# Kernel tuning notes

Hardware: AMD Instinct MI355X
Metric: run time of the kernel (lower is better)

Reference implementation:

```python
import jax, jax.numpy as jnp
import numpy as np

N_NODES = 50000

def gcn_conv(x, src, dst, W, b):
    # x: [N, F_in], src/dst: [E], W: [F_in, F_out], b: [F_out]
    n = x.shape[0]
    xw = x @ W  # [N, F_out]
    # degree including self-loop (counted on destination nodes, PyG convention)
    deg = jax.ops.segment_sum(jnp.ones(src.shape[0], xw.dtype), dst, num_segments=n) + 1.0
    dinv = jax.lax.rsqrt(deg)  # deg >= 1 always
    norm = dinv[src] * dinv[dst]  # [E]
    msgs = xw[src] * norm[:, None]  # [E, F_out] gather + scale
    agg = jax.ops.segment_sum(msgs, dst, num_segments=n)  # scatter-add
    agg = agg + xw * (dinv * dinv)[:, None]  # self-loop contribution
    return agg + b


def setup_inputs() -> dict:
    key = jax.random.key(0)
    ks = jax.random.split(key, 8)
    n, e = N_NODES, 800000
    c_in, c_hid, c_out = 128, 128, 64
    x = jax.random.normal(ks[0], (n, c_in), dtype=jnp.float32)
    edge_index = jax.random.randint(ks[1], (2, e), 0, n, dtype=jnp.int64)
    s = 1.0 / np.sqrt(c_in)
    W1 = jax.random.uniform(ks[2], (c_in, c_hid), jnp.float32, -s, s)
    b1 = jnp.zeros((c_hid,), jnp.float32)
    sh = 1.0 / np.sqrt(c_hid)
    W2 = jax.random.uniform(ks[3], (c_hid, c_hid), jnp.float32, -sh, sh)
    b2 = jnp.zeros((c_hid,), jnp.float32)
    W3 = jax.random.uniform(ks[4], (c_hid, c_out), jnp.float32, -sh, sh)
    b3 = jnp.zeros((c_out,), jnp.float32)
    return {"x": x, "edge_index": edge_index, "W1": W1, "b1": b1,
            "W2": W2, "b2": b2, "W3": W3, "b3": b3}


def reference(x, edge_index, W1, b1, W2, b2, W3, b3):
    src, dst = edge_index[0], edge_index[1]
    h = gcn_conv(x, src, dst, W1, b1)
    h = gcn_conv(h, src, dst, W2, b2)
    h = gcn_conv(h, src, dst, W3, b3)
    return jax.nn.relu(h)  # activation applied after last layer only
```

## Files before the change

### kernel.cpp

```cpp
#include <hip/hip_runtime.h>
#include <hip/hip_fp16.h>


#define C_IN 128
#define C_HID 128
#define C_OUT 64
#define PART_BLOCKS 256

typedef __attribute__((ext_vector_type(8))) short bf16x8;
typedef __attribute__((ext_vector_type(4))) float f32x4;

__device__ __forceinline__ unsigned short bf16_rne(float f) {
    unsigned u = __float_as_uint(f);
    unsigned r = u + 0x7FFFu + ((u >> 16) & 1u);
    return (unsigned short)(r >> 16);
}
__device__ __forceinline__ float bf16_f(unsigned short h) {
    return __uint_as_float(((unsigned)h) << 16);
}


__global__ __launch_bounds__(256) void buk_hist_kernel(const int* __restrict__ dst, int E,
                                                       int* __restrict__ bukCnt) {
    __shared__ int h[256];
    int tid = threadIdx.x;
    h[tid] = 0;
    __syncthreads();
    int chunk = (E + gridDim.x - 1) / gridDim.x;
    int lo = blockIdx.x * chunk;
    int hi = min(lo + chunk, E);
    for (int e = lo + tid; e < hi; e += 256)
        atomicAdd(&h[dst[e] >> 8], 1);
    __syncthreads();
    if (h[tid] > 0) atomicAdd(&bukCnt[tid], h[tid]);
}

__global__ __launch_bounds__(256) void buk_scan_kernel(const int* __restrict__ bukCnt,
                                                       int nbuk, int E,
                                                       int* __restrict__ bbase,
                                                       int* __restrict__ cursor) {
    __shared__ int lds[256];
    int tid = threadIdx.x;
    int v = (tid < nbuk) ? bukCnt[tid] : 0;
    lds[tid] = v;
    __syncthreads();
    for (int off = 1; off < 256; off <<= 1) {
        int u = (tid >= off) ? lds[tid - off] : 0;
        __syncthreads();
        lds[tid] += u;
        __syncthreads();
    }
    int ex = lds[tid] - v;
    if (tid < nbuk) { bbase[tid] = ex; cursor[tid] = ex; }
    if (tid == 0) bbase[nbuk] = E;
}

__global__ __launch_bounds__(256) void buk_place_kernel(const int* __restrict__ src,
                                                        const int* __restrict__ dst, int E,
                                                        int* __restrict__ cursor,
                                                        int2* __restrict__ ebuf) {
    __shared__ int h[256];
    __shared__ int base[256];
    __shared__ int c2[256];
    int tid = threadIdx.x;
    h[tid] = 0;
    c2[tid] = 0;
    __syncthreads();
    int chunk = (E + gridDim.x - 1) / gridDim.x;
    int lo = blockIdx.x * chunk;
    int hi = min(lo + chunk, E);
    for (int e = lo + tid; e < hi; e += 256)
        atomicAdd(&h[dst[e] >> 8], 1);
    __syncthreads();
    int cnt = h[tid];
    if (cnt > 0) base[tid] = atomicAdd(&cursor[tid], cnt);
    __syncthreads();
    for (int e = lo + tid; e < hi; e += 256) {
        int d = dst[e];
        int b = d >> 8;
        int slot = base[b] + atomicAdd(&c2[b], 1);
        ebuf[slot] = make_int2(src[e], d);
    }
}

__global__ __launch_bounds__(256) void buk_fill_kernel(const int2* __restrict__ ebuf,
                                                       const int* __restrict__ bbase,
                                                       int n, int E,
                                                       int* __restrict__ rowptr,
                                                       float* __restrict__ dinv,
                                                       int* __restrict__ csr) {
    __shared__ int deg[256];
    __shared__ int lds[256];
    int b = blockIdx.x;
    int tid = threadIdx.x;
    int lo = bbase[b];
    int hi = bbase[b + 1];
    int node0 = b << 8;
    deg[tid] = 0;
    __syncthreads();
    for (int e = lo + tid; e < hi; e += 256)
        atomicAdd(&deg[ebuf[e].y & 255], 1);
    __syncthreads();
    int d = deg[tid];
    lds[tid] = d;
    __syncthreads();
    for (int off = 1; off < 256; off <<= 1) {
        int u = (tid >= off) ? lds[tid - off] : 0;
        __syncthreads();
        lds[tid] += u;
        __syncthreads();
    }
    int ex = lds[tid] - d;
    int node = node0 + tid;
    if (node < n) {
        rowptr[node] = lo + ex;
        dinv[node] = rsqrtf((float)d + 1.0f);
    }
    if (tid == 0)
        rowptr[min(node0 + 256, n)] = hi;
    __syncthreads();
    deg[tid] = lo + ex;
    __syncthreads();
    for (int e = lo + tid; e < hi; e += 256) {
        int2 ed = ebuf[e];
        int slot = atomicAdd(&deg[ed.y & 255], 1);
        csr[slot] = ed.x;
    }
}

__global__ __launch_bounds__(256) void split_kernel(const float* __restrict__ X,
                                                    unsigned short* __restrict__ Hi,
                                                    unsigned short* __restrict__ Lo,
                                                    int total4) {
    int g = blockIdx.x * blockDim.x + threadIdx.x;
    if (g >= total4) return;
    float4 v = ((const float4*)X)[g];
    float vv[4] = {v.x, v.y, v.z, v.w};
    unsigned short h[4], l[4];
#pragma unroll
    for (int i = 0; i < 4; ++i) {
        h[i] = bf16_rne(vv[i]);
        l[i] = bf16_rne(vv[i] - bf16_f(h[i]));
    }
    uint2 ph = make_uint2((unsigned)h[0] | ((unsigned)h[1] << 16),
                          (unsigned)h[2] | ((unsigned)h[3] << 16));
    uint2 pl = make_uint2((unsigned)l[0] | ((unsigned)l[1] << 16),
                          (unsigned)l[2] | ((unsigned)l[3] << 16));
    ((uint2*)Hi)[g] = ph;
    ((uint2*)Lo)[g] = pl;
}

__global__ __launch_bounds__(256) void wsplit_all_kernel(const float* __restrict__ W1,
                                                         const float* __restrict__ W2,
                                                         const float* __restrict__ W3,
                                                         unsigned short* __restrict__ Wf) {
    int g = blockIdx.x * 256 + threadIdx.x;
    const float* W;
    int FOUT, NF, base;
    if (g < 2048)      { W = W1; FOUT = 128; NF = 2048; base = 0;     }
    else if (g < 4096) { W = W2; FOUT = 128; NF = 2048; base = 32768; g -= 2048; }
    else if (g < 5120) { W = W3; FOUT = 64;  NF = 1024; base = 65536; g -= 4096; }
    else return;
    int lane = g & 63;
    int nt = (g >> 6) & 3;
    int kt = (g >> 8) & 3;
    int ct = g >> 10;
    int kbase = kt * 32 + (lane >> 4) * 8;
    int cc = ct * 64 + nt * 16 + (lane & 15);
    unsigned short hi8[8], lo8[8];
#pragma unroll
    for (int j = 0; j < 8; ++j) {
        float w = W[(size_t)(kbase + j) * FOUT + cc];
        hi8[j] = bf16_rne(w);
        lo8[j] = bf16_rne(w - bf16_f(hi8[j]));
    }
    *(bf16x8*)&Wf[(size_t)(base + g * 8)] = *(bf16x8*)hi8;
    *(bf16x8*)&Wf[(size_t)(base + NF * 8 + g * 8)] = *(bf16x8*)lo8;
}

template <int FOUT>
__global__ __launch_bounds__(256, 3) void gemm_mfma(const unsigned short* __restrict__ Xhi,
                                                    const unsigned short* __restrict__ Xlo,
                                                    const unsigned short* __restrict__ WfHi,
                                                    const unsigned short* __restrict__ WfLo,
                                                    const float* __restrict__ dinv,
                                                    float* __restrict__ Y,
                                                    __half* __restrict__ Yh, int n) {
    constexpr int CTILES = FOUT / 64;
    int tid = threadIdx.x;
    int wv = tid >> 6, lane = tid & 63;
    int ct = (CTILES == 1) ? 0 : (blockIdx.x % CTILES);
    int rt = blockIdx.x / CTILES;
    int col0 = ct * 64;
    int row0 = rt * 64 + wv * 16;

    int rA = row0 + (lane & 15);
    if (rA > n - 1) rA = n - 1;
    const unsigned short* ph = Xhi + (size_t)rA * 128 + ((lane >> 4) * 8);
    const unsigned short* pl = Xlo + (size_t)rA * 128 + ((lane >> 4) * 8);
    bf16x8 ah[4], al[4];
#pragma unroll
    for (int kt = 0; kt < 4; ++kt) {
        ah[kt] = *(const bf16x8*)(ph + kt * 32);
        al[kt] = *(const bf16x8*)(pl + kt * 32);
    }

    const bf16x8* bhp = (const bf16x8*)WfHi + (size_t)ct * 1024 + lane;
    const bf16x8* blp = (const bf16x8*)WfLo + (size_t)ct * 1024 + lane;

    f32x4 acc[4];
#pragma unroll
    for (int nt = 0; nt < 4; ++nt) acc[nt] = (f32x4){0.f, 0.f, 0.f, 0.f};

#pragma unroll
    for (int kt = 0; kt < 4; ++kt) {
        bf16x8 bh[4], bl[4];
#pragma unroll
        for (int nt = 0; nt < 4; ++nt) {
            bh[nt] = bhp[(kt * 4 + nt) * 64];
            bl[nt] = blp[(kt * 4 + nt) * 64];
        }
#pragma unroll
        for (int nt = 0; nt < 4; ++nt) {
            acc[nt] = __builtin_amdgcn_mfma_f32_16x16x32_bf16(ah[kt], bh[nt], acc[nt], 0, 0, 0);
            acc[nt] = __builtin_amdgcn_mfma_f32_16x16x32_bf16(ah[kt], bl[nt], acc[nt], 0, 0, 0);
            acc[nt] = __builtin_amdgcn_mfma_f32_16x16x32_bf16(al[kt], bh[nt], acc[nt], 0, 0, 0);
        }
    }

#pragma unroll
    for (int r = 0; r < 4; ++r) {
        int grow = row0 + (lane >> 4) * 4 + r;
        if (grow < n) {
            float di = dinv[grow];
#pragma unroll
            for (int nt = 0; nt < 4; ++nt) {
                float v = acc[nt][r];
                size_t off = (size_t)grow * FOUT + col0 + nt * 16 + (lane & 15);
                Y[off] = v;
                Yh[off] = __float2half(v * di);
            }
        }
    }
}

template <int NB, bool MASK>
__device__ __forceinline__ void batch_f128(const int* __restrict__ csr, int j, int rem,
                                           const __half* __restrict__ xwh, int lane,
                                           float2* acc) {
    int s[NB];
#pragma unroll
    for (int k = 0; k < NB; ++k) {
        int jj = MASK ? (j + ((k < rem) ? k : 0)) : (j + k);
        s[k] = csr[jj];
    }
    float2 v[NB];
#pragma unroll
    for (int k = 0; k < NB; ++k) {
        __half2 hv = ((const __half2*)(xwh + (size_t)s[k] * 128))[lane];
        v[k] = __half22float2(hv);
    }
#pragma unroll
    for (int k = 0; k < NB; ++k) {
        float m = (!MASK || (k < rem)) ? 1.0f : 0.0f;
        acc[k & 3].x = fmaf(v[k].x, m, acc[k & 3].x);
        acc[k & 3].y = fmaf(v[k].y, m, acc[k & 3].y);
    }
}

template <int NB, bool MASK>
__device__ __forceinline__ void batch_f64(const int* __restrict__ csr, int j, int rem,
                                          const __half* __restrict__ xwh, int lane,
                                          float* acc) {
    int s[NB];
#pragma unroll
    for (int k = 0; k < NB; ++k) {
        int jj = MASK ? (j + ((k < rem) ? k : 0)) : (j + k);
        s[k] = csr[jj];
    }
    float v[NB];
#pragma unroll
    for (int k = 0; k < NB; ++k)
        v[k] = __half2float(xwh[(size_t)s[k] * 64 + lane]);
#pragma unroll
    for (int k = 0; k < NB; ++k) {
        float m = (!MASK || (k < rem)) ? 1.0f : 0.0f;
        acc[k & 3] = fmaf(v[k], m, acc[k & 3]);
    }
}

template <int F, int MODE>
__global__ __launch_bounds__(256) void agg_kernel(const int* __restrict__ rowptr,
                                                  const int* __restrict__ csr,
                                                  const float* __restrict__ xw,
                                                  const __half* __restrict__ xwh,
                                                  const float* __restrict__ dinv,
                                                  const float* __restrict__ bias,
                                                  float* __restrict__ out,
                                                  unsigned short* __restrict__ outHi,
                                                  unsigned short* __restrict__ outLo,
                                                  int n) {
    int wave = threadIdx.x >> 6;
    int lane = threadIdx.x & 63;
    int i0 = blockIdx.x * 4 + wave;
    if (i0 >= n) return;
    int i = __builtin_amdgcn_readfirstlane(i0);
    float di = dinv[i];
    float d2 = di * di;
    int j = rowptr[i];
    int end = rowptr[i + 1];
    j = __builtin_amdgcn_readfirstlane(j);
    end = __builtin_amdgcn_readfirstlane(end);

    if constexpr (F == 128) {
        float2 x0 = ((const float2*)(xw + (size_t)i * F))[lane];
        float2 acc[4];
        acc[0] = acc[1] = acc[2] = acc[3] = make_float2(0.f, 0.f);

        for (; j + 16 <= end; j += 16) batch_f128<16, false>(csr, j, 0, xwh, lane, acc);
        if (j + 8 <= end) { batch_f128<8, false>(csr, j, 0, xwh, lane, acc); j += 8; }
        if (j + 4 <= end) { batch_f128<4, false>(csr, j, 0, xwh, lane, acc); j += 4; }
        int rem = end - j;
        if (rem > 0) batch_f128<4, true>(csr, j, rem, xwh, lane, acc);

        float2 bv = ((const float2*)bias)[lane];
        float ox = fmaf(di, (acc[0].x + acc[1].x) + (acc[2].x + acc[3].x),
                        fmaf(x0.x, d2, bv.x));
        float oy = fmaf(di, (acc[0].y + acc[1].y) + (acc[2].y + acc[3].y),
                        fmaf(x0.y, d2, bv.y));
        unsigned short h0 = bf16_rne(ox);
        unsigned short l0 = bf16_rne(ox - bf16_f(h0));
        unsigned short h1 = bf16_rne(oy);
        unsigned short l1 = bf16_rne(oy - bf16_f(h1));
        ((unsigned*)(outHi + (size_t)i * F))[lane] = (unsigned)h0 | ((unsigned)h1 << 16);
        ((unsigned*)(outLo + (size_t)i * F))[lane] = (unsigned)l0 | ((unsigned)l1 << 16);
    } else {
        float x0 = xw[(size_t)i * F + lane];
        float acc[4] = {0.f, 0.f, 0.f, 0.f};

        for (; j + 16 <= end; j += 16) batch_f64<16, false>(csr, j, 0, xwh, lane, acc);
        if (j + 8 <= end) { batch_f64<8, false>(csr, j, 0, xwh, lane, acc); j += 8; }
        if (j + 4 <= end) { batch_f64<4, false>(csr, j, 0, xwh, lane, acc); j += 4; }
        int rem = end - j;
        if (rem > 0) batch_f64<4, true>(csr, j, rem, xwh, lane, acc);

        float o = fmaf(di, (acc[0] + acc[1]) + (acc[2] + acc[3]),
                       fmaf(x0, d2, bias[lane]));
        o = fmaxf(o, 0.f);
        out[(size_t)i * F + lane] = o;
    }
}

extern "C" void kernel_launch(void* const* d_in, const int* in_sizes, int n_in,
                              void* d_out, int out_size, void* d_ws, size_t ws_size,
                              hipStream_t stream) {
    const float* x  = (const float*)d_in[0];
    const int*   ei = (const int*)d_in[1];
    const float* W1 = (const float*)d_in[2];
    const float* b1 = (const float*)d_in[3];
    const float* W2 = (const float*)d_in[4];
    const float* b2 = (const float*)d_in[5];
    const float* W3 = (const float*)d_in[6];
    const float* b3 = (const float*)d_in[7];
    float* out = (float*)d_out;

    int E = in_sizes[1] / 2;
    int n = in_sizes[0] / C_IN;
    const int* src = ei;
    const int* dst = ei + E;
    int nbuk = (n + 255) >> 8;

    float*          A    = (float*)d_ws;
    __half*         Ah   = (__half*)(A + (size_t)n * C_HID);
    unsigned short* Bhi  = (unsigned short*)(Ah + (size_t)n * C_HID);
    unsigned short* Blo  = Bhi + (size_t)n * C_HID;
    unsigned short* Wf   = Blo + (size_t)n * C_HID;
    int2*           ebuf = (int2*)(Wf + 81920);
    int*            csr  = (int*)(ebuf + E);
    float*          dinv = (float*)(csr + E);
    int*            rowptr = (int*)(dinv + n);
    int*            bukCnt = rowptr + n + 1;
    int*            bbase  = bukCnt + 256;
    int*            cursor = bbase + 256 + 1;

    unsigned short* W1h = Wf;
    unsigned short* W1l = Wf + 16384;
    unsigned short* W2h = Wf + 32768;
    unsigned short* W2l = Wf + 49152;
    unsigned short* W3h = Wf + 65536;
    unsigned short* W3l = Wf + 73728;

    hipMemsetAsync(bukCnt, 0, 256 * sizeof(int), stream);
    buk_hist_kernel<<<PART_BLOCKS, 256, 0, stream>>>(dst, E, bukCnt);
    buk_scan_kernel<<<1, 256, 0, stream>>>(bukCnt, nbuk, E, bbase, cursor);
    buk_place_kernel<<<PART_BLOCKS, 256, 0, stream>>>(src, dst, E, cursor, ebuf);
    buk_fill_kernel<<<nbuk, 256, 0, stream>>>(ebuf, bbase, n, E, rowptr, dinv, csr);

    wsplit_all_kernel<<<20, 256, 0, stream>>>(W1, W2, W3, Wf);
    int total4 = n * C_IN / 4;
    split_kernel<<<(total4 + 255) / 256, 256, 0, stream>>>(x, Bhi, Blo, total4);

    int aggBlocks = (n + 3) / 4;
    int rowTiles = (n + 63) / 64;

    gemm_mfma<C_HID><<<rowTiles * 2, 256, 0, stream>>>(Bhi, Blo, W1h, W1l, dinv, A, Ah, n);
    agg_kernel<C_HID, 0><<<aggBlocks, 256, 0, stream>>>(rowptr, csr, A, Ah, dinv, b1,
                                                        nullptr, Bhi, Blo, n);
    gemm_mfma<C_HID><<<rowTiles * 2, 256, 0, stream>>>(Bhi, Blo, W2h, W2l, dinv, A, Ah, n);
    agg_kernel<C_HID, 0><<<aggBlocks, 256, 0, stream>>>(rowptr, csr, A, Ah, dinv, b2,
                                                        nullptr, Bhi, Blo, n);
    gemm_mfma<C_OUT><<<rowTiles, 256, 0, stream>>>(Bhi, Blo, W3h, W3l, dinv, A, Ah, n);
    agg_kernel<C_OUT, 1><<<aggBlocks, 256, 0, stream>>>(rowptr, csr, A, Ah, dinv, b3,
                                                        out, nullptr, nullptr, n);
}
```

Before: 278.3 us.

## Fuse aggregation with next-layer GEMM and fold input bf16 split into GEMM1

Drops the standalone split kernel: the first GEMM now reads fp32 x and splits it into bf16 hi/lo in registers. Each layer-1 and layer-2 aggregation is fused with the following layer's MFMA GEMM. Aggregated rows go into a 64-row LDS tile and are multiplied directly, so the hi/lo activation buffers are never written to or re-read from global memory. This removes two launches and intermediate traffic. In exchange each block runs only 4 waves over 64 nodes with a 33KB LDS tile, which lowers parallelism and latency hiding for the irregular gather phase. It also double-buffers the Y arrays.

```diff
diff --git a/kernel.cpp b/kernel.cpp
--- a/kernel.cpp
+++ b/kernel.cpp
@@ -126,28 +126,6 @@
         int slot = atomicAdd(&deg[ed.y & 255], 1);
         csr[slot] = ed.x;
     }
-}
-
-__global__ __launch_bounds__(256) void split_kernel(const float* __restrict__ X,
-                                                    unsigned short* __restrict__ Hi,
-                                                    unsigned short* __restrict__ Lo,
-                                                    int total4) {
-    int g = blockIdx.x * blockDim.x + threadIdx.x;
-    if (g >= total4) return;
-    float4 v = ((const float4*)X)[g];
-    float vv[4] = {v.x, v.y, v.z, v.w};
-    unsigned short h[4], l[4];
-#pragma unroll
-    for (int i = 0; i < 4; ++i) {
-        h[i] = bf16_rne(vv[i]);
-        l[i] = bf16_rne(vv[i] - bf16_f(h[i]));
-    }
-    uint2 ph = make_uint2((unsigned)h[0] | ((unsigned)h[1] << 16),
-                          (unsigned)h[2] | ((unsigned)h[3] << 16));
-    uint2 pl = make_uint2((unsigned)l[0] | ((unsigned)l[1] << 16),
-                          (unsigned)l[2] | ((unsigned)l[3] << 16));
-    ((uint2*)Hi)[g] = ph;
-    ((uint2*)Lo)[g] = pl;
 }
 
 __global__ __launch_bounds__(256) void wsplit_all_kernel(const float* __restrict__ W1,
@@ -178,31 +156,39 @@
     *(bf16x8*)&Wf[(size_t)(base + NF * 8 + g * 8)] = *(bf16x8*)lo8;
 }
 
-template <int FOUT>
-__global__ __launch_bounds__(256, 3) void gemm_mfma(const unsigned short* __restrict__ Xhi,
-                                                    const unsigned short* __restrict__ Xlo,
-                                                    const unsigned short* __restrict__ WfHi,
-                                                    const unsigned short* __restrict__ WfLo,
-                                                    const float* __restrict__ dinv,
-                                                    float* __restrict__ Y,
-                                                    __half* __restrict__ Yh, int n) {
-    constexpr int CTILES = FOUT / 64;
+__device__ __forceinline__ void split8(const float* v, bf16x8& hv, bf16x8& lv) {
+#pragma unroll
+    for (int j = 0; j < 8; ++j) {
+        unsigned short h = bf16_rne(v[j]);
+        hv[j] = (short)h;
+        lv[j] = (short)bf16_rne(v[j] - bf16_f(h));
+    }
+}
+
+__global__ __launch_bounds__(256, 3) void gemm1_mfma(const float* __restrict__ X,
+                                                     const unsigned short* __restrict__ WfHi,
+                                                     const unsigned short* __restrict__ WfLo,
+                                                     const float* __restrict__ dinv,
+                                                     float* __restrict__ Y,
+                                                     __half* __restrict__ Yh, int n) {
+    constexpr int FOUT = 128;
     int tid = threadIdx.x;
     int wv = tid >> 6, lane = tid & 63;
-    int ct = (CTILES == 1) ? 0 : (blockIdx.x % CTILES);
-    int rt = blockIdx.x / CTILES;
+    int ct = blockIdx.x & 1;
+    int rt = blockIdx.x >> 1;
     int col0 = ct * 64;
     int row0 = rt * 64 + wv * 16;
 
     int rA = row0 + (lane & 15);
     if (rA > n - 1) rA = n - 1;
-    const unsigned short* ph = Xhi + (size_t)rA * 128 + ((lane >> 4) * 8);
-    const unsigned short* pl = Xlo + (size_t)rA * 128 + ((lane >> 4) * 8);
+    const float* px = X + (size_t)rA * 128 + ((lane >> 4) * 8);
     bf16x8 ah[4], al[4];
 #pragma unroll
     for (int kt = 0; kt < 4; ++kt) {
-        ah[kt] = *(const bf16x8*)(ph + kt * 32);
-        al[kt] = *(const bf16x8*)(pl + kt * 32);
+        float v[8];
+        *(float4*)&v[0] = *(const float4*)(px + kt * 32);
+        *(float4*)&v[4] = *(const float4*)(px + kt * 32 + 4);
+        split8(v, ah[kt], al[kt]);
     }
 
     const bf16x8* bhp = (const bf16x8*)WfHi + (size_t)ct * 1024 + lane;
@@ -289,17 +275,114 @@
     }
 }
 
-template <int F, int MODE>
-__global__ __launch_bounds__(256) void agg_kernel(const int* __restrict__ rowptr,
-                                                  const int* __restrict__ csr,
-                                                  const float* __restrict__ xw,
-                                                  const __half* __restrict__ xwh,
-                                                  const float* __restrict__ dinv,
-                                                  const float* __restrict__ bias,
-                                                  float* __restrict__ out,
-                                                  unsigned short* __restrict__ outHi,
-                                                  unsigned short* __restrict__ outLo,
-                                                  int n) {
+template <int FOUT>
+__global__ __launch_bounds__(256, 3) void fused_agg_gemm(const int* __restrict__ rowptr,
+                                                         const int* __restrict__ csr,
+                                                         const float* __restrict__ xw,
+                                                         const __half* __restrict__ xwh,
+                                                         const float* __restrict__ dinv,
+                                                         const float* __restrict__ bias,
+                                                         const unsigned short* __restrict__ WfHi,
+                                                         const unsigned short* __restrict__ WfLo,
+                                                         float* __restrict__ Y,
+                                                         __half* __restrict__ Yh, int n) {
+    constexpr int CTILES = FOUT / 64;
+    __shared__ float hl[64][132];
+
+    int tid = threadIdx.x;
+    int wv = tid >> 6, lane = tid & 63;
+    int node0 = blockIdx.x * 64;
+
+    for (int nn = 0; nn < 16; ++nn) {
+        int nodeLocal = wv * 16 + nn;
+        int i0 = node0 + nodeLocal;
+        if (i0 >= n) {
+            ((float2*)&hl[nodeLocal][0])[lane] = make_float2(0.f, 0.f);
+            continue;
+        }
+        int i = __builtin_amdgcn_readfirstlane(i0);
+        float di = dinv[i];
+        float d2 = di * di;
+        int j = rowptr[i];
+        int end = rowptr[i + 1];
+        j = __builtin_amdgcn_readfirstlane(j);
+        end = __builtin_amdgcn_readfirstlane(end);
+
+        float2 x0 = ((const float2*)(xw + (size_t)i * 128))[lane];
+        float2 acc[4];
+        acc[0] = acc[1] = acc[2] = acc[3] = make_float2(0.f, 0.f);
+        for (; j + 16 <= end; j += 16) batch_f128<16, false>(csr, j, 0, xwh, lane, acc);
+        if (j + 8 <= end) { batch_f128<8, false>(csr, j, 0, xwh, lane, acc); j += 8; }
+        if (j + 4 <= end) { batch_f128<4, false>(csr, j, 0, xwh, lane, acc); j += 4; }
+        int rem = end - j;
+        if (rem > 0) batch_f128<4, true>(csr, j, rem, xwh, lane, acc);
+
+        float2 bv = ((const float2*)bias)[lane];
+        float2 o;
+        o.x = fmaf(di, (acc[0].x + acc[1].x) + (acc[2].x + acc[3].x),
+                   fmaf(x0.x, d2, bv.x));
+        o.y = fmaf(di, (acc[0].y + acc[1].y) + (acc[2].y + acc[3].y),
+                   fmaf(x0.y, d2, bv.y));
+        ((float2*)&hl[nodeLocal][0])[lane] = o;
+    }
+
+    int rowL = wv * 16 + (lane & 15);
+    bf16x8 ah[4], al[4];
+#pragma unroll
+    for (int kt = 0; kt < 4; ++kt) {
+        int cb = kt * 32 + (lane >> 4) * 8;
+        float v[8];
+        *(float4*)&v[0] = *(const float4*)&hl[rowL][cb];
+        *(float4*)&v[4] = *(const float4*)&hl[rowL][cb + 4];
+        split8(v, ah[kt], al[kt]);
+    }
+
+#pragma unroll
+    for (int ct = 0; ct < CTILES; ++ct) {
+        const bf16x8* bhp = (const bf16x8*)WfHi + (size_t)ct * 1024 + lane;
+        const bf16x8* blp = (const bf16x8*)WfLo + (size_t)ct * 1024 + lane;
+        f32x4 acc[4];
+#pragma unroll
+        for (int nt = 0; nt < 4; ++nt) acc[nt] = (f32x4){0.f, 0.f, 0.f, 0.f};
+#pragma unroll
+        for (int kt = 0; kt < 4; ++kt) {
+            bf16x8 bh[4], bl[4];
+#pragma unroll
+            for (int nt = 0; nt < 4; ++nt) {
+                bh[nt] = bhp[(kt * 4 + nt) * 64];
+                bl[nt] = blp[(kt * 4 + nt) * 64];
+            }
+#pragma unroll
+            for (int nt = 0; nt < 4; ++nt) {
+                acc[nt] = __builtin_amdgcn_mfma_f32_16x16x32_bf16(ah[kt], bh[nt], acc[nt], 0, 0, 0);
+                acc[nt] = __builtin_amdgcn_mfma_f32_16x16x32_bf16(ah[kt], bl[nt], acc[nt], 0, 0, 0);
+                acc[nt] = __builtin_amdgcn_mfma_f32_16x16x32_bf16(al[kt], bh[nt], acc[nt], 0, 0, 0);
+            }
+        }
+#pragma unroll
+        for (int r = 0; r < 4; ++r) {
+            int grow = node0 + wv * 16 + (lane >> 4) * 4 + r;
+            if (grow < n) {
+                float di = dinv[grow];
+#pragma unroll
+                for (int nt = 0; nt < 4; ++nt) {
+                    float v = acc[nt][r];
+                    size_t off = (size_t)grow * FOUT + ct * 64 + nt * 16 + (lane & 15);
+                    Y[off] = v;
+                    Yh[off] = __float2half(v * di);
+                }
+            }
+        }
+    }
+}
+
+__global__ __launch_bounds__(256) void agg64_kernel(const int* __restrict__ rowptr,
+                                                    const int* __restrict__ csr,
+                                                    const float* __restrict__ xw,
+                                                    const __half* __restrict__ xwh,
+                                                    const float* __restrict__ dinv,
+                                                    const float* __restrict__ bias,
+                                                    float* __restrict__ out, int n) {
     int wave = threadIdx.x >> 6;
     int lane = threadIdx.x & 63;
     int i0 = blockIdx.x * 4 + wave;
@@ -312,43 +395,18 @@
     j = __builtin_amdgcn_readfirstlane(j);
     end = __builtin_amdgcn_readfirstlane(end);
 
-    if constexpr (F == 128) {
-        float2 x0 = ((const float2*)(xw + (size_t)i * F))[lane];
-        float2 acc[4];
-        acc[0] = acc[1] = acc[2] = acc[3] = make_float2(0.f, 0.f);
-
-        for (; j + 16 <= end; j += 16) batch_f128<16, false>(csr, j, 0, xwh, lane, acc);
-        if (j + 8 <= end) { batch_f128<8, false>(csr, j, 0, xwh, lane, acc); j += 8; }
-        if (j + 4 <= end) { batch_f128<4, false>(csr, j, 0, xwh, lane, acc); j += 4; }
-        int rem = end - j;
-        if (rem > 0) batch_f128<4, true>(csr, j, rem, xwh, lane, acc);
-
-        float2 bv = ((const float2*)bias)[lane];
-        float ox = fmaf(di, (acc[0].x + acc[1].x) + (acc[2].x + acc[3].x),
-                        fmaf(x0.x, d2, bv.x));
-        float oy = fmaf(di, (acc[0].y + acc[1].y) + (acc[2].y + acc[3].y),
-                        fmaf(x0.y, d2, bv.y));
-        unsigned short h0 = bf16_rne(ox);
-        unsigned short l0 = bf16_rne(ox - bf16_f(h0));
-        unsigned short h1 = bf16_rne(oy);
-        unsigned short l1 = bf16_rne(oy - bf16_f(h1));
-        ((unsigned*)(outHi + (size_t)i * F))[lane] = (unsigned)h0 | ((unsigned)h1 << 16);
-        ((unsigned*)(outLo + (size_t)i * F))[lane] = (unsigned)l0 | ((unsigned)l1 << 16);
-    } else {
-        float x0 = xw[(size_t)i * F + lane];
-        float acc[4] = {0.f, 0.f, 0.f, 0.f};
-
-        for (; j + 16 <= end; j += 16) batch_f64<16, false>(csr, j, 0, xwh, lane, acc);
-        if (j + 8 <= end) { batch_f64<8, false>(csr, j, 0, xwh, lane, acc); j += 8; }
-        if (j + 4 <= end) { batch_f64<4, false>(csr, j, 0, xwh, lane, acc); j += 4; }
-        int rem = end - j;
-        if (rem > 0) batch_f64<4, true>(csr, j, rem, xwh, lane, acc);
-
-        float o = fmaf(di, (acc[0] + acc[1]) + (acc[2] + acc[3]),
-                       fmaf(x0, d2, bias[lane]));
-        o = fmaxf(o, 0.f);
-        out[(size_t)i * F + lane] = o;
-    }
+    float x0 = xw[(size_t)i * 64 + lane];
+    float acc[4] = {0.f, 0.f, 0.f, 0.f};
+    for (; j + 16 <= end; j += 16) batch_f64<16, false>(csr, j, 0, xwh, lane, acc);
+    if (j + 8 <= end) { batch_f64<8, false>(csr, j, 0, xwh, lane, acc); j += 8; }
+    if (j + 4 <= end) { batch_f64<4, false>(csr, j, 0, xwh, lane, acc); j += 4; }
+    int rem = end - j;
+    if (rem > 0) batch_f64<4, true>(csr, j, rem, xwh, lane, acc);
+
+    float o = fmaf(di, (acc[0] + acc[1]) + (acc[2] + acc[3]),
+                   fmaf(x0, d2, bias[lane]));
+    o = fmaxf(o, 0.f);
+    out[(size_t)i * 64 + lane] = o;
 }
 
 extern "C" void kernel_launch(void* const* d_in, const int* in_sizes, int n_in,
@@ -370,11 +428,11 @@
     const int* dst = ei + E;
     int nbuk = (n + 255) >> 8;
 
-    float*          A    = (float*)d_ws;
-    __half*         Ah   = (__half*)(A + (size_t)n * C_HID);
-    unsigned short* Bhi  = (unsigned short*)(Ah + (size_t)n * C_HID);
-    unsigned short* Blo  = Bhi + (size_t)n * C_HID;
-    unsigned short* Wf   = Blo + (size_t)n * C_HID;
+    float*          Ya   = (float*)d_ws;
+    __half*         Aha  = (__half*)(Ya + (size_t)n * C_HID);
+    float*          Yb   = (float*)(Aha + (size_t)n * C_HID);
+    __half*         Ahb  = (__half*)(Yb + (size_t)n * C_HID);
+    unsigned short* Wf   = (unsigned short*)(Ahb + (size_t)n * C_HID);
     int2*           ebuf = (int2*)(Wf + 81920);
     int*            csr  = (int*)(ebuf + E);
     float*          dinv = (float*)(csr + E);
@@ -397,19 +455,14 @@
     buk_fill_kernel<<<nbuk, 256, 0, stream>>>(ebuf, bbase, n, E, rowptr, dinv, csr);
 
     wsplit_all_kernel<<<20, 256, 0, stream>>>(W1, W2, W3, Wf);
-    int total4 = n * C_IN / 4;
-    split_kernel<<<(total4 + 255) / 256, 256, 0, stream>>>(x, Bhi, Blo, total4);
-
+
+    int rowTiles = (n + 63) / 64;
     int aggBlocks = (n + 3) / 4;
-    int rowTiles = (n + 63) / 64;
-
-    gemm_mfma<C_HID><<<rowTiles * 2, 256, 0, stream>>>(Bhi, Blo, W1h, W1l, dinv, A, Ah, n);
-    agg_kernel<C_HID, 0><<<aggBlocks, 256, 0, stream>>>(rowptr, csr, A, Ah, dinv, b1,
-                                                        nullptr, Bhi, Blo, n);
-    gemm_mfma<C_HID><<<rowTiles * 2, 256, 0, stream>>>(Bhi, Blo, W2h, W2l, dinv, A, Ah, n);
-    agg_kernel<C_HID, 0><<<aggBlocks, 256, 0, stream>>>(rowptr, csr, A, Ah, dinv, b2,
-                                                        nullptr, Bhi, Blo, n);
-    gemm_mfma<C_OUT><<<rowTiles, 256, 0, stream>>>(Bhi, Blo, W3h, W3l, dinv, A, Ah, n);
-    agg_kernel<C_OUT, 1><<<aggBlocks, 256, 0, stream>>>(rowptr, csr, A, Ah, dinv, b3,
-                                                        out, nullptr, nullptr, n);
-}
+
+    gemm1_mfma<<<rowTiles * 2, 256, 0, stream>>>(x, W1h, W1l, dinv, Ya, Aha, n);
+    fused_agg_gemm<C_HID><<<rowTiles, 256, 0, stream>>>(rowptr, csr, Ya, Aha, dinv, b1,
+                                                        W2h, W2l, Yb, Ahb, n);
+    fused_agg_gemm<C_OUT><<<rowTiles, 256, 0, stream>>>(rowptr, csr, Yb, Ahb, dinv, b2,
+                                                        W3h, W3l, Ya, Aha, n);
+    agg64_kernel<<<aggBlocks, 256, 0, stream>>>(rowptr, csr, Ya, Aha, dinv, b3, out, n);
+}
```

New measurement: 283.3 us. No clear change (+1.8%).
